# Kernel optimization log

Hardware: AMD Instinct MI355X
Metric: run time of the kernel (lower is better)

## Reference

```python
import jax, jax.numpy as jnp
import numpy as np

NUM_HEADS_SPLIT = 12   # hardcoded in einops reduce pattern
NUM_HEADS_SCALE = 8    # num_heads used only for scale computation (module bug, kept faithful)


def setup_inputs() -> dict:
    key = jax.random.key(0)
    ks = jax.random.split(key, 5)
    B, P, D = 32, 577, 768
    return {
        "x": jax.random.normal(ks[0], (B, P, D), dtype=jnp.float32),
        "qkv_w": jax.random.normal(ks[1], (3 * D, D), dtype=jnp.float32) * 0.02,
        "qkv_b": jax.random.normal(ks[2], (3 * D,), dtype=jnp.float32) * 0.02,
        "out_w": jax.random.normal(ks[3], (D, D), dtype=jnp.float32) * 0.02,
        "out_b": jax.random.normal(ks[4], (D,), dtype=jnp.float32) * 0.02,
    }


def reference(x, qkv_w, qkv_b, out_w, out_b):
    B, P, D = x.shape
    h = NUM_HEADS_SPLIT
    s = D // h
    scale = (D // NUM_HEADS_SCALE) ** -0.5  # 96**-0.5, per original code

    # qkv projection: [B, P, 3D]
    qkv = jnp.einsum('bpd,ed->bpe', x, qkv_w) + qkv_b
    # reshape 'b p (c h s) -> b p c h s' (reduce with mean is a pure reshape here)
    qkv = qkv.reshape(B, P, 3, h, s)
    # split order in the original: v, q, k
    v = jnp.transpose(qkv[:, :, 0], (0, 2, 1, 3))  # [B, h, P, s]
    q = jnp.transpose(qkv[:, :, 1], (0, 2, 1, 3))
    k = jnp.transpose(qkv[:, :, 2], (0, 2, 1, 3))

    attn = jnp.einsum('bhps,bhqs->bhpq', q, k) * scale
    attn = jax.nn.softmax(attn, axis=-1)
    out = jnp.einsum('bhpq,bhqs->bhps', attn, v)  # [B, h, P, s]
    out = jnp.transpose(out, (0, 2, 1, 3)).reshape(B, P, D)

    return jnp.einsum('bpd,ed->bpe', out, out_w) + out_b
```

## Files before the change

### kernel.cpp

```cpp
#include <hip/hip_runtime.h>
#include <stdint.h>

typedef __attribute__((ext_vector_type(8))) short short8;
typedef __attribute__((ext_vector_type(4))) float floatx4;

#define DEV static __device__ __forceinline__

constexpr int Bb = 32, Pp = 577, Dd = 768, Hh = 12;
constexpr int M_VALID = Bb * Pp;
constexpr int M_PAD   = 18560;
constexpr int PKV     = 640;
constexpr float SCALE_LOG2E = 0.10206207261596577f * 1.4426950408889634f;

DEV ushort f2b(float f) {
  union { float f; uint32_t u; } c; c.f = f;
  uint32_t u = c.u + 0x7fffu + ((c.u >> 16) & 1u);
  return (ushort)(u >> 16);
}

__global__ void cvt_pad(const float* __restrict__ src, ushort* __restrict__ dst,
                        int n_valid4, int n_total4) {
  const float4* s4 = (const float4*)src;
  for (int i = blockIdx.x * blockDim.x + threadIdx.x; i < n_total4;
       i += gridDim.x * blockDim.x) {
    float4 v = make_float4(0.f, 0.f, 0.f, 0.f);
    if (i < n_valid4) v = s4[i];
    ushort4 o;
    o.x = f2b(v.x); o.y = f2b(v.y); o.z = f2b(v.z); o.w = f2b(v.w);
    ((ushort4*)dst)[i] = o;
  }
}

#define STAGE(bi, kk)                                                          \
  do {                                                                         \
    _Pragma("unroll")                                                          \
    for (int c_ = 0; c_ < 4; ++c_)                                             \
      __builtin_amdgcn_global_load_lds(                                        \
          (const __attribute__((address_space(1))) void*)(gA + c_ * 8 + (kk)), \
          (__attribute__((address_space(3))) void*)(As + (bi)*8192 + c_*2048 + tid*8), \
          16, 0, 0);                                                           \
    _Pragma("unroll")                                                          \
    for (int c_ = 0; c_ < 2; ++c_)                                             \
      __builtin_amdgcn_global_load_lds(                                        \
          (const __attribute__((address_space(1))) void*)(gB + c_ * 16 + (kk)),\
          (__attribute__((address_space(3))) void*)(Bs + (bi)*4096 + c_*2048 + tid*8), \
          16, 0, 0);                                                           \
  } while (0)

template<bool C_F32>
__global__ __launch_bounds__(256, 2) void gemm_bt(
    const ushort* __restrict__ A, int lda,
    const ushort* __restrict__ Bw,
    const float* __restrict__ bias, void* __restrict__ Cout,
    int N, int K, int m_valid, int nt_n)
{
  __shared__ ushort As[3 * 8192];
  __shared__ ushort Bs[3 * 4096];
  const int tid = threadIdx.x;
  const int lane = tid & 63;
  const int w = tid >> 6;
  const int wr = w >> 1, wc = w & 1;
  const int llo = lane & 15, lhi = lane >> 4;

  const int nwg = gridDim.x;
  const int L = blockIdx.x;
  const int q = nwg >> 3, r = nwg & 7;
  const int xcd = L & 7, pos = L >> 3;
  const int wgid = (xcd < r ? xcd * (q + 1) : r * (q + 1) + (xcd - r) * q) + pos;
  const int m0 = (wgid / nt_n) * 256, n0 = (wgid % nt_n) * 128;

  floatx4 acc[8][4];
#pragma unroll
  for (int i = 0; i < 8; ++i)
#pragma unroll
    for (int j = 0; j < 4; ++j) acc[i][j] = floatx4{0.f, 0.f, 0.f, 0.f};

  const ushort* gA = A + ((size_t)m0 + tid) * lda;
  const ushort* gB = Bw + (size_t)(n0 + (tid & 127)) * K + (tid >> 7) * 8;

  STAGE(0, 0);
  STAGE(1, 32);
  int cur = 0;
  for (int kk = 0; kk < K; kk += 32) {
    if (kk + 64 < K) {
      int b2 = cur + 2; if (b2 >= 3) b2 -= 3;
      STAGE(b2, kk + 64);
      asm volatile("s_waitcnt vmcnt(12)" ::: "memory");
    } else if (kk + 32 < K) {
      asm volatile("s_waitcnt vmcnt(6)" ::: "memory");
    } else {
      asm volatile("s_waitcnt vmcnt(0)" ::: "memory");
    }
    __builtin_amdgcn_s_barrier();
    __builtin_amdgcn_sched_barrier(0);

    const ushort* Ab = As + cur * 8192;
    const ushort* Bbp = Bs + cur * 4096;
    short8 af[8], bfr[4];
#pragma unroll
    for (int j = 0; j < 4; ++j)
      bfr[j] = *(const short8*)(Bbp + lhi * 1024 + (wc * 64 + j * 16 + llo) * 8);
#pragma unroll
    for (int i = 0; i < 8; ++i)
      af[i] = *(const short8*)(Ab + lhi * 2048 + (wr * 128 + i * 16 + llo) * 8);
#pragma unroll
    for (int i = 0; i < 8; ++i)
#pragma unroll
      for (int j = 0; j < 4; ++j)
        acc[i][j] = __builtin_amdgcn_mfma_f32_16x16x32_bf16(af[i], bfr[j], acc[i][j], 0, 0, 0);

    __builtin_amdgcn_sched_barrier(0);
    __builtin_amdgcn_s_barrier();
    cur += 1; if (cur >= 3) cur -= 3;
  }

  float bv[4];
#pragma unroll
  for (int j = 0; j < 4; ++j) bv[j] = bias[n0 + wc * 64 + j * 16 + llo];

#pragma unroll
  for (int i = 0; i < 8; ++i) {
#pragma unroll
    for (int r2 = 0; r2 < 4; ++r2) {
      const int row = m0 + wr * 128 + i * 16 + lhi * 4 + r2;
      if (row >= m_valid) continue;
      const size_t rb = (size_t)row * N + n0 + wc * 64;
#pragma unroll
      for (int j = 0; j < 4; ++j) {
        float v = acc[i][j][r2] + bv[j];
        if (C_F32) ((float*)Cout)[rb + j * 16 + llo] = v;
        else       ((ushort*)Cout)[rb + j * 16 + llo] = f2b(v);
      }
    }
  }
}

__global__ __launch_bounds__(256) void vtrans(const ushort* __restrict__ C1,
                                              ushort* __restrict__ Vt) {
  const int pt = blockIdx.x, h = blockIdx.y, b = blockIdx.z;
  __shared__ ushort Ts[64][72];
  const int t = threadIdx.x;
  const int rl = t >> 2, c16 = (t & 3) * 16;
  const int p = pt * 64 + rl;
  short8 a0 = {0,0,0,0,0,0,0,0}, a1 = {0,0,0,0,0,0,0,0};
  if (p < Pp) {
    const ushort* s = C1 + (size_t)(b * Pp + p) * 2304 + h * 64 + c16;
    a0 = *(const short8*)s;
    a1 = *(const short8*)(s + 8);
  }
  *(short8*)&Ts[rl][c16] = a0;
  *(short8*)&Ts[rl][c16 + 8] = a1;
  __syncthreads();
  const int ss = t >> 2, pc16 = (t & 3) * 16;
  short8 o0, o1;
#pragma unroll
  for (int i = 0; i < 8; ++i) {
    o0[i] = (short)Ts[pc16 + i][ss];
    o1[i] = (short)Ts[pc16 + 8 + i][ss];
  }
  ushort* d = Vt + ((size_t)(b * Hh + h) * 64 + ss) * PKV + pt * 64 + pc16;
  *(short8*)d = o0;
  *(short8*)(d + 8) = o1;
}

__global__ __launch_bounds__(512) void attn_fwd(
    ushort* C1, const ushort* __restrict__ Vt)
{
  const int qt = blockIdx.x, h = blockIdx.y, b = blockIdx.z;
  const int tid = threadIdx.x;
  const int lane = tid & 63, w = tid >> 6;
  const int llo = lane & 15, lhi = lane >> 4;

  __shared__ ushort Ks[64][72];
  __shared__ ushort Vs[64][72];
  __shared__ ushort Ps[8][16][72];

  const int q0 = qt * 128;
  const int qrow = q0 + w * 16 + llo;
  const size_t qoff = (size_t)(b * Pp + qrow) * 2304 + 768 + h * 64;
  const short8 qf0 = *(const short8*)(C1 + qoff + lhi * 8);
  const short8 qf1 = *(const short8*)(C1 + qoff + 32 + lhi * 8);

  float ls[4] = {0.f, 0.f, 0.f, 0.f};
  floatx4 acc_o[4];
#pragma unroll
  for (int st = 0; st < 4; ++st) acc_o[st] = floatx4{0.f, 0.f, 0.f, 0.f};

  const int srow = tid >> 3;
  const int sc8 = (tid & 7) * 8;
  const ushort* kbase = C1 + (size_t)(b * Pp + srow) * 2304 + 1536 + h * 64 + sc8;
  const ushort* vbase = Vt + ((size_t)(b * Hh + h) * 64 + srow) * PKV + sc8;

  short8 kc = *(const short8*)(kbase);
  short8 vc = *(const short8*)(vbase);

  for (int t = 0; t < 10; ++t) {
    __syncthreads();
    *(short8*)&Ks[srow][sc8] = kc;
    *(short8*)&Vs[srow][sc8] = vc;
    if (t < 9) {
      kc = *(const short8*)(kbase + (size_t)(t + 1) * 64 * 2304);
      vc = *(const short8*)(vbase + (t + 1) * 64);
    }
    __syncthreads();

    float pv[4][4];
#pragma unroll
    for (int ntl = 0; ntl < 4; ++ntl) {
      floatx4 acc = floatx4{0.f, 0.f, 0.f, 0.f};
      const short8 bf0 = *(const short8*)&Ks[ntl * 16 + llo][lhi * 8];
      const short8 bf1 = *(const short8*)&Ks[ntl * 16 + llo][32 + lhi * 8];
      acc = __builtin_amdgcn_mfma_f32_16x16x32_bf16(qf0, bf0, acc, 0, 0, 0);
      acc = __builtin_amdgcn_mfma_f32_16x16x32_bf16(qf1, bf1, acc, 0, 0, 0);
      const bool valid = (t * 64 + ntl * 16 + llo) < Pp;
#pragma unroll
      for (int r = 0; r < 4; ++r) {
        const float p = valid ? exp2f(acc[r] * SCALE_LOG2E) : 0.f;
        pv[ntl][r] = p;
        ls[r] += p;
      }
    }

#pragma unroll
    for (int r = 0; r < 4; ++r)
#pragma unroll
      for (int ntl = 0; ntl < 4; ++ntl)
        Ps[w][lhi * 4 + r][ntl * 16 + llo] = f2b(pv[ntl][r]);

    const short8 pa0 = *(const short8*)&Ps[w][llo][lhi * 8];
    const short8 pa1 = *(const short8*)&Ps[w][llo][32 + lhi * 8];
#pragma unroll
    for (int st = 0; st < 4; ++st) {
      const short8 vb0 = *(const short8*)&Vs[st * 16 + llo][lhi * 8];
      const short8 vb1 = *(const short8*)&Vs[st * 16 + llo][32 + lhi * 8];
      acc_o[st] = __builtin_amdgcn_mfma_f32_16x16x32_bf16(pa0, vb0, acc_o[st], 0, 0, 0);
      acc_o[st] = __builtin_amdgcn_mfma_f32_16x16x32_bf16(pa1, vb1, acc_o[st], 0, 0, 0);
    }
  }

#pragma unroll
  for (int r = 0; r < 4; ++r) {
#pragma unroll
    for (int off = 1; off < 16; off <<= 1) ls[r] += __shfl_xor(ls[r], off, 64);
  }

#pragma unroll
  for (int r = 0; r < 4; ++r) {
    const int p = q0 + w * 16 + lhi * 4 + r;
    if (p < Pp) {
      const float inv = 1.f / ls[r];
      const size_t ob = (size_t)(b * Pp + p) * 2304 + h * 64;
#pragma unroll
      for (int st = 0; st < 4; ++st)
        C1[ob + st * 16 + llo] = f2b(acc_o[st][r] * inv);
    }
  }
}

extern "C" void kernel_launch(void* const* d_in, const int* in_sizes, int n_in,
                              void* d_out, int out_size, void* d_ws, size_t ws_size,
                              hipStream_t stream) {
  const float* x     = (const float*)d_in[0];
  const float* qkv_w = (const float*)d_in[1];
  const float* qkv_b = (const float*)d_in[2];
  const float* out_w = (const float*)d_in[3];
  const float* out_b = (const float*)d_in[4];
  float* out = (float*)d_out;

  char* ws = (char*)d_ws;
  ushort* Xb  = (ushort*)(ws);
  ushort* W1b = (ushort*)(ws + 28508160);
  ushort* C1b = (ushort*)(ws + 32047104);
  ushort* W3b = (ushort*)(ws + 117571584);
  ushort* Vtb = (ushort*)(ws);

  cvt_pad<<<2048, 256, 0, stream>>>(x, Xb, M_VALID * 768 / 4, M_PAD * 768 / 4);
  cvt_pad<<<1024, 256, 0, stream>>>(qkv_w, W1b, 2304 * 768 / 4, 2304 * 768 / 4);
  cvt_pad<<<512, 256, 0, stream>>>(out_w, W3b, 768 * 768 / 4, 768 * 768 / 4);

  gemm_bt<false><<<dim3(73 * 18), 256, 0, stream>>>(Xb, 768, W1b, qkv_b,
                                                    (void*)C1b, 2304, 768, M_PAD, 18);
  vtrans<<<dim3(10, 12, 32), 256, 0, stream>>>(C1b, Vtb);
  attn_fwd<<<dim3(5, 12, 32), 512, 0, stream>>>(C1b, Vtb);
  gemm_bt<true><<<dim3(73 * 6), 256, 0, stream>>>(C1b, 2304, W3b, out_b,
                                                  (void*)out, 768, 768, M_VALID, 6);
}
```

Baseline: 417.1 us.

## Replace GEMM with 8-wave 256x256 tile kernel using swizzled LDS and phased pipeline

Measured after the change: 341.6 us. -18.1%, faster.

```diff
diff --git a/kernel.cpp b/kernel.cpp
--- a/kernel.cpp
+++ b/kernel.cpp
@@ -5,6 +5,8 @@
 typedef __attribute__((ext_vector_type(4))) float floatx4;
 
 #define DEV static __device__ __forceinline__
+#define AS1 __attribute__((address_space(1)))
+#define AS3 __attribute__((address_space(3)))
 
 constexpr int Bb = 32, Pp = 577, Dd = 768, Hh = 12;
 constexpr int M_VALID = Bb * Pp;
@@ -31,35 +33,58 @@
   }
 }
 
-#define STAGE(bi, kk)                                                          \
+#define STAGEHALF(BUF, KH, STK)                                                \
   do {                                                                         \
-    _Pragma("unroll")                                                          \
-    for (int c_ = 0; c_ < 4; ++c_)                                             \
-      __builtin_amdgcn_global_load_lds(                                        \
-          (const __attribute__((address_space(1))) void*)(gA + c_ * 8 + (kk)), \
-          (__attribute__((address_space(3))) void*)(As + (bi)*8192 + c_*2048 + tid*8), \
-          16, 0, 0);                                                           \
-    _Pragma("unroll")                                                          \
-    for (int c_ = 0; c_ < 2; ++c_)                                             \
-      __builtin_amdgcn_global_load_lds(                                        \
-          (const __attribute__((address_space(1))) void*)(gB + c_ * 16 + (kk)),\
-          (__attribute__((address_space(3))) void*)(Bs + (bi)*4096 + c_*2048 + tid*8), \
-          16, 0, 0);                                                           \
+    __builtin_amdgcn_global_load_lds(                                          \
+        (const AS1 void*)(gAs + (STK) + (KH) * 32),                            \
+        (AS3 void*)(As + (BUF) * 16384 + (KH) * 8192 + tid * 8), 16, 0, 0);    \
+    __builtin_amdgcn_global_load_lds(                                          \
+        (const AS1 void*)(gAs + (size_t)128 * lda + (STK) + (KH) * 32),        \
+        (AS3 void*)(As + (BUF) * 16384 + (KH) * 8192 + 4096 + tid * 8), 16, 0, 0); \
+    __builtin_amdgcn_global_load_lds(                                          \
+        (const AS1 void*)(gBs + (STK) + (KH) * 32),                            \
+        (AS3 void*)(Bs_ + (BUF) * 16384 + (KH) * 8192 + tid * 8), 16, 0, 0);   \
+    __builtin_amdgcn_global_load_lds(                                          \
+        (const AS1 void*)(gBs + (size_t)128 * 768 + (STK) + (KH) * 32),        \
+        (AS3 void*)(Bs_ + (BUF) * 16384 + (KH) * 8192 + 4096 + tid * 8), 16, 0, 0); \
   } while (0)
 
+#define PHASE(BUF, KH, STK)                                                    \
+  do {                                                                         \
+    const ushort* Ar = As + (BUF) * 16384 + (KH) * 8192;                       \
+    const ushort* Br = Bs_ + (BUF) * 16384 + (KH) * 8192;                      \
+    short8 af[8], bf[4];                                                       \
+    _Pragma("unroll") for (int j = 0; j < 4; ++j)                              \
+      bf[j] = *(const short8*)(Br + (wn * 64 + j * 16 + llo) * 32 + csw);      \
+    _Pragma("unroll") for (int i = 0; i < 8; ++i)                              \
+      af[i] = *(const short8*)(Ar + (wr * 128 + i * 16 + llo) * 32 + csw);     \
+    asm volatile("s_waitcnt lgkmcnt(0)" ::: "memory");                         \
+    __builtin_amdgcn_sched_barrier(0);                                         \
+    __builtin_amdgcn_s_setprio(1);                                             \
+    _Pragma("unroll") for (int i = 0; i < 8; ++i)                              \
+      _Pragma("unroll") for (int j = 0; j < 4; ++j)                            \
+        acc[i][j] = __builtin_amdgcn_mfma_f32_16x16x32_bf16(af[i], bf[j], acc[i][j], 0, 0, 0); \
+    __builtin_amdgcn_s_setprio(0);                                             \
+    __builtin_amdgcn_sched_barrier(0);                                         \
+    __builtin_amdgcn_s_barrier();                \
+    STAGEHALF(BUF, KH, STK);                     \
+    asm volatile("s_waitcnt vmcnt(12)" ::: "memory");                          \
+    __builtin_amdgcn_s_barrier();                \
+  } while (0)
+
 template<bool C_F32>
-__global__ __launch_bounds__(256, 2) void gemm_bt(
+__global__ __launch_bounds__(512, 2) void gemm8p(
     const ushort* __restrict__ A, int lda,
     const ushort* __restrict__ Bw,
     const float* __restrict__ bias, void* __restrict__ Cout,
-    int N, int K, int m_valid, int nt_n)
+    int N, int m_valid, int nt_n)
 {
-  __shared__ ushort As[3 * 8192];
-  __shared__ ushort Bs[3 * 4096];
+  __shared__ ushort As[32768];
+  __shared__ ushort Bs_[32768];
   const int tid = threadIdx.x;
   const int lane = tid & 63;
   const int w = tid >> 6;
-  const int wr = w >> 1, wc = w & 1;
+  const int wr = w >> 2, wn = w & 3;
   const int llo = lane & 15, lhi = lane >> 4;
 
   const int nwg = gridDim.x;
@@ -67,7 +92,7 @@
   const int q = nwg >> 3, r = nwg & 7;
   const int xcd = L & 7, pos = L >> 3;
   const int wgid = (xcd < r ? xcd * (q + 1) : r * (q + 1) + (xcd - r) * q) + pos;
-  const int m0 = (wgid / nt_n) * 256, n0 = (wgid % nt_n) * 128;
+  const int m0 = (wgid / nt_n) * 256, n0 = (wgid % nt_n) * 256;
 
   floatx4 acc[8][4];
 #pragma unroll
@@ -75,48 +100,32 @@
 #pragma unroll
     for (int j = 0; j < 4; ++j) acc[i][j] = floatx4{0.f, 0.f, 0.f, 0.f};
 
-  const ushort* gA = A + ((size_t)m0 + tid) * lda;
-  const ushort* gB = Bw + (size_t)(n0 + (tid & 127)) * K + (tid >> 7) * 8;
-
-  STAGE(0, 0);
-  STAGE(1, 32);
-  int cur = 0;
-  for (int kk = 0; kk < K; kk += 32) {
-    if (kk + 64 < K) {
-      int b2 = cur + 2; if (b2 >= 3) b2 -= 3;
-      STAGE(b2, kk + 64);
-      asm volatile("s_waitcnt vmcnt(12)" ::: "memory");
-    } else if (kk + 32 < K) {
-      asm volatile("s_waitcnt vmcnt(6)" ::: "memory");
-    } else {
-      asm volatile("s_waitcnt vmcnt(0)" ::: "memory");
-    }
-    __builtin_amdgcn_s_barrier();
-    __builtin_amdgcn_sched_barrier(0);
-
-    const ushort* Ab = As + cur * 8192;
-    const ushort* Bbp = Bs + cur * 4096;
-    short8 af[8], bfr[4];
-#pragma unroll
-    for (int j = 0; j < 4; ++j)
-      bfr[j] = *(const short8*)(Bbp + lhi * 1024 + (wc * 64 + j * 16 + llo) * 8);
-#pragma unroll
-    for (int i = 0; i < 8; ++i)
-      af[i] = *(const short8*)(Ab + lhi * 2048 + (wr * 128 + i * 16 + llo) * 8);
-#pragma unroll
-    for (int i = 0; i < 8; ++i)
-#pragma unroll
-      for (int j = 0; j < 4; ++j)
-        acc[i][j] = __builtin_amdgcn_mfma_f32_16x16x32_bf16(af[i], bfr[j], acc[i][j], 0, 0, 0);
-
-    __builtin_amdgcn_sched_barrier(0);
-    __builtin_amdgcn_s_barrier();
-    cur += 1; if (cur >= 3) cur -= 3;
+  const int sg = ((tid & 3) ^ ((tid >> 3) & 3)) * 8;
+  const ushort* gAs = A  + (size_t)(m0 + (tid >> 2)) * lda + sg;
+  const ushort* gBs = Bw + (size_t)(n0 + (tid >> 2)) * 768 + sg;
+  const int csw = (lhi ^ ((llo >> 1) & 3)) * 8;
+
+  STAGEHALF(0, 0, 0);
+  STAGEHALF(0, 1, 0);
+  STAGEHALF(1, 0, 64);
+  STAGEHALF(1, 1, 64);
+  asm volatile("s_waitcnt vmcnt(8)" ::: "memory");
+  __builtin_amdgcn_s_barrier();
+
+#pragma unroll 1
+  for (int m = 0; m < 6; ++m) {
+    const int t2 = 2 * m + 2, t3 = 2 * m + 3;
+    const int s0 = (t2 < 12 ? t2 : 11) * 64;
+    const int s1 = (t3 < 12 ? t3 : 11) * 64;
+    PHASE(0, 0, s0);
+    PHASE(0, 1, s0);
+    PHASE(1, 0, s1);
+    PHASE(1, 1, s1);
   }
 
   float bv[4];
 #pragma unroll
-  for (int j = 0; j < 4; ++j) bv[j] = bias[n0 + wc * 64 + j * 16 + llo];
+  for (int j = 0; j < 4; ++j) bv[j] = bias[n0 + wn * 64 + j * 16 + llo];
 
 #pragma unroll
   for (int i = 0; i < 8; ++i) {
@@ -124,7 +133,7 @@
     for (int r2 = 0; r2 < 4; ++r2) {
       const int row = m0 + wr * 128 + i * 16 + lhi * 4 + r2;
       if (row >= m_valid) continue;
-      const size_t rb = (size_t)row * N + n0 + wc * 64;
+      const size_t rb = (size_t)row * N + n0 + wn * 64;
 #pragma unroll
       for (int j = 0; j < 4; ++j) {
         float v = acc[i][j][r2] + bv[j];
@@ -278,10 +287,10 @@
   cvt_pad<<<1024, 256, 0, stream>>>(qkv_w, W1b, 2304 * 768 / 4, 2304 * 768 / 4);
   cvt_pad<<<512, 256, 0, stream>>>(out_w, W3b, 768 * 768 / 4, 768 * 768 / 4);
 
-  gemm_bt<false><<<dim3(73 * 18), 256, 0, stream>>>(Xb, 768, W1b, qkv_b,
-                                                    (void*)C1b, 2304, 768, M_PAD, 18);
+  gemm8p<false><<<dim3(73 * 9), 512, 0, stream>>>(Xb, 768, W1b, qkv_b,
+                                                  (void*)C1b, 2304, M_PAD, 9);
   vtrans<<<dim3(10, 12, 32), 256, 0, stream>>>(C1b, Vtb);
   attn_fwd<<<dim3(5, 12, 32), 512, 0, stream>>>(C1b, Vtb);
-  gemm_bt<true><<<dim3(73 * 6), 256, 0, stream>>>(C1b, 2304, W3b, out_b,
-                                                  (void*)out, 768, 768, M_VALID, 6);
-}
+  gemm8p<true><<<dim3(73 * 3), 512, 0, stream>>>(C1b, 2304, W3b, out_b,
+                                                 (void*)out, 768, M_VALID, 3);
+}
```
